# Performance work log

Measured on AMD Instinct MI355X. Metric: run time of the kernel, lower is better.

## Reference

```python
import jax, jax.numpy as jnp
import numpy as np

BATCH = 16384
N_IN = 128
CTX = 128
H = 1024
NB = 8                      # num_bins
OUT_MULT = 3 * NB - 1       # widths + heights + derivatives for RQS
TAIL = 3.0                  # tail_bound
SCALE = float(np.sqrt((H * H) // 2))  # sqrt(prod(hidden_dims)//len(hidden_dims))
MIN_W = 1e-3; MIN_H = 1e-3; MIN_D = 1e-3
DPAD = float(np.log(np.exp(1.0 - MIN_D) - 1.0))  # softplus(DPAD)+MIN_D == 1 at boundaries


def _masks():
    # Standard sequential MADE masks. Input degrees 1..n_in, hidden degrees cycle.
    deg_in = np.arange(1, N_IN + 1)
    deg_h = (np.arange(H) % (N_IN - 1)) + 1
    m0 = deg_h[:, None] >= deg_in[None, :]          # [H, N_IN]
    m1 = deg_h[:, None] >= deg_h[None, :]           # [H, H]
    deg_out = np.repeat(deg_in, OUT_MULT)           # matches view(b, n_in, out_mult)
    m2 = deg_out[:, None] > deg_h[None, :]          # [N_IN*OUT_MULT, H]
    return jnp.asarray(m0), jnp.asarray(m1), jnp.asarray(m2)


def setup_inputs() -> dict:
    key = jax.random.key(0)
    k = jax.random.split(key, 6)
    def rn(kk, shape, fan_in):
        return (jax.random.normal(kk, shape, dtype=jnp.float32) * np.sqrt(1.0 / fan_in)).astype(jnp.float32)
    m0, m1, m2 = _masks()
    return {
        "x": jax.random.normal(k[0], (BATCH, N_IN), dtype=jnp.float32),
        "context": jax.random.normal(k[1], (BATCH, CTX), dtype=jnp.float32),
        "ctx_w": rn(k[2], (H, CTX), CTX),
        "w0": rn(k[3], (H, N_IN), N_IN), "b0": jnp.zeros((H,), jnp.float32),
        "w1": rn(k[4], (H, H), H),       "b1": jnp.zeros((H,), jnp.float32),
        "w2": rn(k[5], (N_IN * OUT_MULT, H), H), "b2": jnp.zeros((N_IN * OUT_MULT,), jnp.float32),
        "mask0": m0, "mask1": m1, "mask2": m2,
    }


def _rqs(x, uw, uh, ud):
    # x: [B, D]; uw, uh: [B, D, NB]; ud: [B, D, NB-1]
    inside = jnp.abs(x) <= TAIL
    xc = jnp.clip(x, -TAIL, TAIL)

    w = MIN_W + (1.0 - MIN_W * NB) * jax.nn.softmax(uw, axis=-1)
    cw = jnp.cumsum(w, axis=-1)
    cw = jnp.concatenate([jnp.zeros_like(cw[..., :1]), cw], axis=-1)
    cw = 2.0 * TAIL * cw - TAIL
    cw = cw.at[..., 0].set(-TAIL).at[..., -1].set(TAIL)
    widths = cw[..., 1:] - cw[..., :-1]

    h = MIN_H + (1.0 - MIN_H * NB) * jax.nn.softmax(uh, axis=-1)
    ch = jnp.cumsum(h, axis=-1)
    ch = jnp.concatenate([jnp.zeros_like(ch[..., :1]), ch], axis=-1)
    ch = 2.0 * TAIL * ch - TAIL
    ch = ch.at[..., 0].set(-TAIL).at[..., -1].set(TAIL)
    heights = ch[..., 1:] - ch[..., :-1]

    pad = jnp.full(ud.shape[:-1] + (1,), DPAD, ud.dtype)
    d = MIN_D + jax.nn.softplus(jnp.concatenate([pad, ud, pad], axis=-1))  # [B, D, NB+1]

    # bucketize: bin index per element (NB is small; comparison-sum beats searchsorted here)
    idx = jnp.clip(jnp.sum((xc[..., None] >= cw).astype(jnp.int32), axis=-1) - 1, 0, NB - 1)
    g = lambda a, i: jnp.take_along_axis(a, i[..., None], axis=-1)[..., 0]

    in_cw = g(cw, idx); in_w = g(widths, idx)
    in_ch = g(ch, idx); in_h = g(heights, idx)
    delta = in_h / in_w
    d0 = g(d, idx); d1 = g(d, idx + 1)

    theta = (xc - in_cw) / in_w
    t1m = theta * (1.0 - theta)
    denom = delta + (d0 + d1 - 2.0 * delta) * t1m
    num = in_h * (delta * theta * theta + d0 * t1m)
    y = in_ch + num / denom
    logdet = (2.0 * jnp.log(delta)
              + jnp.log(d1 * theta * theta + 2.0 * delta * t1m + d0 * (1.0 - theta) ** 2)
              - 2.0 * jnp.log(denom))

    y = jnp.where(inside, y, x)          # identity linear tails
    logdet = jnp.where(inside, logdet, 0.0)
    return y, logdet


def reference(x, context, ctx_w, w0, b0, w1, b1, w2, b2, mask0, mask1, mask2):
    m0 = mask0.astype(w0.dtype); m1 = mask1.astype(w1.dtype); m2 = mask2.astype(w2.dtype)
    hdn = jax.nn.relu(context @ ctx_w.T + x @ (w0 * m0).T + b0)
    hdn = jax.nn.relu(hdn @ (w1 * m1).T + b1)
    out = (hdn @ (w2 * m2).T + b2).reshape(-1, N_IN, OUT_MULT)
    uw = out[..., :NB] / SCALE
    uh = out[..., NB:2 * NB] / SCALE
    ud = out[..., 2 * NB:]
    y, ld = _rqs(x, uw, uh, ud)
    return y, jnp.sum(ld, axis=-1)
```

## Files before the change

### kernel.cpp

```cpp
#include <hip/hip_runtime.h>
#include <cstdint>
#include <cstddef>

#define BATCH   16384
#define N_IN    128
#define CTX     128
#define HDIM    1024
#define NB      8
#define OUT_MULT 23
#define OUT_PAD 24
#define NOUTP   (N_IN * OUT_PAD)
#define KCAT    (CTX + N_IN)

typedef __bf16 bf16x8 __attribute__((ext_vector_type(8)));
typedef float  f32x4  __attribute__((ext_vector_type(4)));

__device__ __forceinline__ uint16_t f2bf(float f) {
    union { float f; uint32_t u; } v; v.f = f;
    uint32_t u = v.u;
    u += 0x7FFFu + ((u >> 16) & 1u);
    return (uint16_t)(u >> 16);
}

__device__ __forceinline__ int kpref_dev(int d) {
    return (d <= 8) ? 9 * d : 72 + 8 * (d - 8);
}
__device__ __forceinline__ int dpos_dev(int p) {
    return (p < 72) ? (p / 9) : (8 + ((p - 72) >> 3));
}
__device__ __forceinline__ int h_of(int p) {
    if (p < 72) { int d = p / 9, j = p - 9 * d; return d + 127 * j; }
    int q = p - 72; int d = 8 + (q >> 3); int j = q & 7; return d + 127 * j;
}

__device__ __forceinline__ void async_ld16(const void* g, const void* l) {
    __builtin_amdgcn_global_load_lds(
        (__attribute__((address_space(1))) void*)(uintptr_t)g,
        (__attribute__((address_space(3))) void*)(uint32_t)(uintptr_t)l,
        16, 0, 0);
}


__global__ void pack_all(
    const float* __restrict__ x,    const float* __restrict__ ctx,
    const float* __restrict__ ctx_w,const float* __restrict__ w0,
    const float* __restrict__ b0,   const float* __restrict__ w1,
    const float* __restrict__ b1,   const float* __restrict__ w2,
    const float* __restrict__ b2,
    uint16_t* __restrict__ xcat, uint16_t* __restrict__ wcat,
    uint16_t* __restrict__ w1m,  uint16_t* __restrict__ w2p,
    float* __restrict__ b0p, float* __restrict__ b1p, float* __restrict__ b2p,
    float* __restrict__ ldz)
{
    const int blk = blockIdx.x;
    const int tid = threadIdx.x;
    if (blk < 16384) {
        int idx = blk * 256 + tid;
        int b = idx >> 8, c = idx & 255;
        float v = (c < CTX) ? ctx[(b << 7) + c] : x[(b << 7) + (c - CTX)];
        xcat[idx] = f2bf(v);
    } else if (blk < 17408) {
        int idx = (blk - 16384) * 256 + tid;
        int p = idx >> 8, c = idx & 255;
        int h = h_of(p);
        float v;
        if (c < CTX) v = ctx_w[(h << 7) + c];
        else {
            int col = c - CTX;
            v = (dpos_dev(p) >= col) ? w0[(h << 7) + col] : 0.0f;
        }
        wcat[idx] = f2bf(v);
    } else if (blk < 21504) {
        int idx = (blk - 17408) * 256 + tid;
        int po = idx >> 10, pi = idx & 1023;
        float v = (dpos_dev(po) >= dpos_dev(pi))
                ? w1[h_of(po) * HDIM + h_of(pi)] : 0.0f;
        w1m[idx] = f2bf(v);
    } else if (blk < 33792) {
        int idx = (blk - 21504) * 256 + tid;
        int oo = idx >> 10, pi = idx & 1023;
        int g = oo / OUT_PAD, t = oo - g * OUT_PAD;
        float v = (t < OUT_MULT && g > dpos_dev(pi))
                ? w2[(g * OUT_MULT + t) * HDIM + h_of(pi)] : 0.0f;
        w2p[idx] = f2bf(v);
    } else if (blk < 33808) {
        int idx = (blk - 33792) * 256 + tid;
        if (idx < HDIM) {
            int h = h_of(idx);
            b0p[idx] = b0[h];
            b1p[idx] = b1[h];
        } else {
            int oo = idx - HDIM;
            int g = oo / OUT_PAD, t = oo - g * OUT_PAD;
            b2p[oo] = (t < OUT_MULT) ? b2[g * OUT_MULT + t] : 0.0f;
        }
    } else {
        int idx = (blk - 33808) * 256 + tid;
        ldz[idx] = 0.0f;
    }
}


template<int MODE>
__global__ __launch_bounds__(256, 2) void gemm_bt(
    const uint16_t* __restrict__ A,
    const uint16_t* __restrict__ B,
    const float*    __restrict__ bias,
    uint16_t*       __restrict__ C,
    int N, int K, int NT)
{
    __shared__ __align__(16) uint16_t sA[128 * 32];
    __shared__ __align__(16) uint16_t sB[128 * 32];

    const int GM    = 64;
    const int per   = GM * NT;
    const int id    = blockIdx.x;
    const int grp   = id / per;
    const int rem   = id - grp * per;
    const int mt    = grp * GM + (rem & (GM - 1));
    const int nt    = rem >> 6;
    const int bm    = mt << 7;
    const int bn    = nt << 7;

    int K_eff;
    if (MODE == 0)      { int dmax = dpos_dev(bn + 127); K_eff = 128 + dmax + 1; }
    else                { int dmax = dpos_dev(bn + 127); K_eff = kpref_dev(dmax + 1); }
    K_eff = min(K, (K_eff + 31) & ~31);

    const int tid   = threadIdx.x;
    const int wid   = tid >> 6;
    const int lane  = tid & 63;
    const int wm    = (wid & 1) << 6;
    const int wn    = (wid >> 1) << 6;
    const int lrow  = lane & 15;
    const int lquad = lane >> 4;

    const f32x4 vzero = {0.0f, 0.0f, 0.0f, 0.0f};
    f32x4 acc[4][4];
#pragma unroll
    for (int i = 0; i < 4; ++i)
#pragma unroll
        for (int j = 0; j < 4; ++j) acc[i][j] = vzero;

    const int c0 = (wid << 6) + lane;
    const int c1 = c0 + 256;
    const char* gA = (const char*)(A + (size_t)bm * K);
    const char* gB = (const char*)(B + (size_t)bn * K);
    const size_t ga0 = (size_t)(c0 >> 2) * K * 2 + (size_t)(c0 & 3) * 16;
    const size_t ga1 = (size_t)(c1 >> 2) * K * 2 + (size_t)(c1 & 3) * 16;
    const char* lA0 = (const char*)sA + (size_t)(wid << 6) * 16;
    const char* lA1 = lA0 + 256 * 16;
    const char* lB0 = (const char*)sB + (size_t)(wid << 6) * 16;
    const char* lB1 = lB0 + 256 * 16;

    const uint16_t* rA = sA + (wm + lrow) * 32 + lquad * 8;
    const uint16_t* rB = sB + (wn + lrow) * 32 + lquad * 8;

    for (int k0 = 0; k0 < K_eff; k0 += 32) {
        __syncthreads();
        const size_t kb = (size_t)k0 * 2;
        async_ld16(gA + ga0 + kb, lA0);
        async_ld16(gA + ga1 + kb, lA1);
        async_ld16(gB + ga0 + kb, lB0);
        async_ld16(gB + ga1 + kb, lB1);
        __syncthreads();

        bf16x8 af[4], bfr[4];
#pragma unroll
        for (int i = 0; i < 4; ++i) af[i]  = *(const bf16x8*)(rA + i * 16 * 32);
#pragma unroll
        for (int j = 0; j < 4; ++j) bfr[j] = *(const bf16x8*)(rB + j * 16 * 32);
#pragma unroll
        for (int i = 0; i < 4; ++i)
#pragma unroll
            for (int j = 0; j < 4; ++j)
                acc[i][j] = __builtin_amdgcn_mfma_f32_16x16x32_bf16(
                                af[i], bfr[j], acc[i][j], 0, 0, 0);
    }

#pragma unroll
    for (int j = 0; j < 4; ++j) {
        const int col = bn + wn + j * 16 + lrow;
        const float bv = bias[col];
#pragma unroll
        for (int i = 0; i < 4; ++i) {
            const int row0 = bm + wm + i * 16 + (lquad << 2);
#pragma unroll
            for (int r = 0; r < 4; ++r) {
                float v = fmaxf(acc[i][j][r] + bv, 0.0f);
                C[(size_t)(row0 + r) * N + col] = f2bf(v);
            }
        }
    }
}


__device__ __forceinline__ float frcp(float v) { return __builtin_amdgcn_rcpf(v); }
__device__ __forceinline__ float softplusf(float v) {
    return fmaxf(v, 0.0f) + __logf(1.0f + __expf(-fabsf(v)));
}

__device__ __forceinline__ void spline_eval(const float* __restrict__ pp,
                                            float xv, float& yout, float& ldout)
{
    float p[OUT_MULT];
#pragma unroll
    for (int k = 0; k < OUT_MULT; ++k) p[k] = pp[k];

    const float TAILF = 3.0f;
    const float MIN_W = 0.001f, MIN_H = 0.001f, MIN_D = 0.001f;
    const float INV_SCALE = 1.0f / 724.0773439350246f;

    const float xc = fminf(fmaxf(xv, -TAILF), TAILF);

    float uw[NB], uh[NB];
#pragma unroll
    for (int k = 0; k < NB; ++k) { uw[k] = p[k] * INV_SCALE; uh[k] = p[NB + k] * INV_SCALE; }
    float mw = uw[0], mh = uh[0];
#pragma unroll
    for (int k = 1; k < NB; ++k) { mw = fmaxf(mw, uw[k]); mh = fmaxf(mh, uh[k]); }
    float ew[NB], eh[NB], sw = 0.0f, sh = 0.0f;
#pragma unroll
    for (int k = 0; k < NB; ++k) {
        ew[k] = __expf(uw[k] - mw); sw += ew[k];
        eh[k] = __expf(uh[k] - mh); sh += eh[k];
    }
    const float FACW = (1.0f - MIN_W * NB) * frcp(sw);
    const float FACH = (1.0f - MIN_H * NB) * frcp(sh);

    float cw[NB + 1], ch[NB + 1];
    cw[0] = -TAILF; ch[0] = -TAILF;
    float aw = 0.0f, ah = 0.0f;
#pragma unroll
    for (int k = 0; k < NB; ++k) {
        aw += MIN_W + FACW * ew[k];
        ah += MIN_H + FACH * eh[k];
        cw[k + 1] = (k == NB - 1) ? TAILF : 2.0f * TAILF * aw - TAILF;
        ch[k + 1] = (k == NB - 1) ? TAILF : 2.0f * TAILF * ah - TAILF;
    }

    float dd[NB + 1];
    dd[0]  = 1.0f;
    dd[NB] = 1.0f;
#pragma unroll
    for (int k = 1; k < NB; ++k) dd[k] = MIN_D + softplusf(p[2 * NB + (k - 1)]);

    float in_cw = cw[0], cw_n = cw[1], in_ch = ch[0], ch_n = ch[1];
    float d0 = dd[0], d1 = dd[1];
#pragma unroll
    for (int k = 1; k < NB; ++k) {
        const bool ge = (xc >= cw[k]);
        in_cw = ge ? cw[k]     : in_cw;
        cw_n  = ge ? cw[k + 1] : cw_n;
        in_ch = ge ? ch[k]     : in_ch;
        ch_n  = ge ? ch[k + 1] : ch_n;
        d0    = ge ? dd[k]     : d0;
        d1    = ge ? dd[k + 1] : d1;
    }
    const float in_w  = cw_n - in_cw;
    const float in_h  = ch_n - in_ch;
    const float inv_w = frcp(in_w);
    const float delta = in_h * inv_w;
    const float theta = (xc - in_cw) * inv_w;
    const float omt   = 1.0f - theta;
    const float t1m   = theta * omt;
    const float denom = delta + (d0 + d1 - 2.0f * delta) * t1m;
    const float num   = in_h * (delta * theta * theta + d0 * t1m);
    float yv = in_ch + num * frcp(denom);
    float ld = 2.0f * __logf(delta)
             + __logf(d1 * theta * theta + 2.0f * delta * t1m + d0 * omt * omt)
             - 2.0f * __logf(denom);
    const bool inside = fabsf(xv) <= TAILF;
    yout  = inside ? yv : xv;
    ldout = inside ? ld : 0.0f;
}


__global__ __launch_bounds__(256, 2) void gemm3_spline(
    const uint16_t* __restrict__ A,
    const uint16_t* __restrict__ B,
    const float*    __restrict__ bias,
    const float*    __restrict__ x,
    float* __restrict__ y,
    float* __restrict__ ldsum)
{
    __shared__ __align__(16) char smem[64 * 97 * 4];
    uint16_t* sA = (uint16_t*)smem;
    uint16_t* sB = (uint16_t*)(smem + 8192);
    float* ep    = (float*)smem;

    const int NT  = 32;
    const int per = 64 * NT;
    const int id  = blockIdx.x;
    const int grp = id / per;
    const int rem = id - grp * per;
    const int mt  = grp * 64 + (rem & 63);
    const int nt  = rem >> 6;
    const int bm  = mt << 7;
    const int bn  = nt * 96;

    const int K = HDIM;
    int K_eff = kpref_dev(4 * nt + 3);
    K_eff = min(K, (K_eff + 31) & ~31);

    const int tid   = threadIdx.x;
    const int wid   = tid >> 6;
    const int lane  = tid & 63;
    const int wm    = (wid & 1) << 6;
    const int wn    = (wid >> 1) * 48;
    const int lrow  = lane & 15;
    const int lquad = lane >> 4;

    const f32x4 vzero = {0.0f, 0.0f, 0.0f, 0.0f};
    f32x4 acc[4][3];
#pragma unroll
    for (int i = 0; i < 4; ++i)
#pragma unroll
        for (int j = 0; j < 3; ++j) acc[i][j] = vzero;

    const int cA0 = (wid << 6) + lane;
    const int cA1 = cA0 + 256;
    const int cB1 = 256 + (wid << 6) + lane;
    const char* gA = (const char*)(A + (size_t)bm * K);
    const char* gB = (const char*)(B + (size_t)bn * K);
    const size_t gaA0 = (size_t)(cA0 >> 2) * K * 2 + (size_t)(cA0 & 3) * 16;
    const size_t gaA1 = (size_t)(cA1 >> 2) * K * 2 + (size_t)(cA1 & 3) * 16;
    const size_t gaB0 = gaA0;
    const size_t gaB1 = (size_t)(cB1 >> 2) * K * 2 + (size_t)(cB1 & 3) * 16;
    const char* lA0 = (const char*)sA + (size_t)(wid << 6) * 16;
    const char* lA1 = lA0 + 256 * 16;
    const char* lB0 = (const char*)sB + (size_t)(wid << 6) * 16;
    const char* lB1 = (const char*)sB + 4096 + (size_t)(wid << 6) * 16;

    const uint16_t* rA = sA + (wm + lrow) * 32 + lquad * 8;
    const uint16_t* rB = sB + (wn + lrow) * 32 + lquad * 8;

    for (int k0 = 0; k0 < K_eff; k0 += 32) {
        __syncthreads();
        const size_t kb = (size_t)k0 * 2;
        async_ld16(gA + gaA0 + kb, lA0);
        async_ld16(gA + gaA1 + kb, lA1);
        async_ld16(gB + gaB0 + kb, lB0);
        if (wid < 2) async_ld16(gB + gaB1 + kb, lB1);
        __syncthreads();

        bf16x8 af[4], bfr[3];
#pragma unroll
        for (int i = 0; i < 4; ++i) af[i]  = *(const bf16x8*)(rA + i * 16 * 32);
#pragma unroll
        for (int j = 0; j < 3; ++j) bfr[j] = *(const bf16x8*)(rB + j * 16 * 32);
#pragma unroll
        for (int i = 0; i < 4; ++i)
#pragma unroll
            for (int j = 0; j < 3; ++j)
                acc[i][j] = __builtin_amdgcn_mfma_f32_16x16x32_bf16(
                                af[i], bfr[j], acc[i][j], 0, 0, 0);
    }

    const int srow = tid >> 2;
    const int sg   = tid & 3;
#pragma unroll
    for (int e = 0; e < 2; ++e) {
        __syncthreads();
        if (wm == (e << 6)) {
#pragma unroll
            for (int j = 0; j < 3; ++j) {
                const int col = wn + j * 16 + lrow;
                const float bv = bias[bn + col];
#pragma unroll
                for (int i = 0; i < 4; ++i) {
                    const int r0 = i * 16 + (lquad << 2);
#pragma unroll
                    for (int r = 0; r < 4; ++r)
                        ep[(r0 + r) * 97 + col] = acc[i][j][r] + bv;
                }
            }
        }
        __syncthreads();

        const int grow = bm + (e << 6) + srow;
        const float xv = x[(size_t)grow * N_IN + (4 * nt + sg)];
        float yv, ld;
        spline_eval(ep + srow * 97 + sg * OUT_PAD, xv, yv, ld);
        y[(size_t)grow * N_IN + 4 * nt + sg] = yv;

        ld += __shfl_xor(ld, 1, 64);
        ld += __shfl_xor(ld, 2, 64);
        if (sg == 0) atomicAdd(&ldsum[grow], ld);
    }
}


extern "C" void kernel_launch(void* const* d_in, const int* in_sizes, int n_in,
                              void* d_out, int out_size, void* d_ws, size_t ws_size,
                              hipStream_t stream)
{
    const float* x     = (const float*)d_in[0];
    const float* ctx   = (const float*)d_in[1];
    const float* ctx_w = (const float*)d_in[2];
    const float* w0    = (const float*)d_in[3];
    const float* b0    = (const float*)d_in[4];
    const float* w1    = (const float*)d_in[5];
    const float* b1    = (const float*)d_in[6];
    const float* w2    = (const float*)d_in[7];
    const float* b2    = (const float*)d_in[8];

    char* ws = (char*)d_ws;
    const size_t XCAT_B = (size_t)BATCH * KCAT * 2;
    const size_t H_B    = (size_t)BATCH * HDIM * 2;
    const size_t WCAT_B = (size_t)HDIM * KCAT * 2;
    const size_t W1_B   = (size_t)HDIM * HDIM * 2;
    const size_t W2P_B  = (size_t)NOUTP * HDIM * 2;

    uint16_t* xcat = (uint16_t*)(ws);
    uint16_t* h1   = (uint16_t*)(ws + XCAT_B);
    uint16_t* h2   = (uint16_t*)(ws + XCAT_B + H_B);
    uint16_t* wcat = (uint16_t*)(ws + XCAT_B + 2 * H_B);
    uint16_t* w1m  = (uint16_t*)(ws + XCAT_B + 2 * H_B + WCAT_B);
    uint16_t* w2p  = (uint16_t*)(ws + XCAT_B + 2 * H_B + WCAT_B + W1_B);
    float*    b0p  = (float*)   (ws + XCAT_B + 2 * H_B + WCAT_B + W1_B + W2P_B);
    float*    b1p  = b0p + HDIM;
    float*    b2p  = b1p + HDIM;

    float* yout  = (float*)d_out;
    float* ldout = yout + (size_t)BATCH * N_IN;

    pack_all<<<33872, 256, 0, stream>>>(x, ctx, ctx_w, w0, b0, w1, b1, w2, b2,
                                        xcat, wcat, w1m, w2p, b0p, b1p, b2p,
                                        ldout);

    const dim3 blk(256);
    gemm_bt<0><<<dim3(128 * (HDIM / 128)), blk, 0, stream>>>(
        xcat, wcat, b0p, h1, HDIM, KCAT, HDIM / 128);
    gemm_bt<1><<<dim3(128 * (HDIM / 128)), blk, 0, stream>>>(
        h1, w1m, b1p, h2, HDIM, HDIM, HDIM / 128);
    gemm3_spline<<<dim3(128 * 32), blk, 0, stream>>>(
        h2, w2p, b2p, x, yout, ldout);
}
```

Measured before the change: 247.9 us.

## Double K-tile depth to 64 with XOR-swizzled LDS layout in GEMM kernels

Both GEMM kernels now stage a 64-wide K slice per iteration instead of 32, which halves the number of barrier pairs and global-to-LDS load rounds. The LDS rows are laid out with an XOR swizzle of the 16-byte chunk index by row, so the fragment reads avoid bank conflicts. The cost is doubled LDS per block and K_eff rounded up to a multiple of 64, which may add some wasted MFMA work on masked-prefix tiles.

```diff
diff --git a/kernel.cpp b/kernel.cpp
--- a/kernel.cpp
+++ b/kernel.cpp
@@ -109,8 +109,8 @@
     uint16_t*       __restrict__ C,
     int N, int K, int NT)
 {
-    __shared__ __align__(16) uint16_t sA[128 * 32];
-    __shared__ __align__(16) uint16_t sB[128 * 32];
+    __shared__ __align__(16) uint16_t sA[128 * 64];
+    __shared__ __align__(16) uint16_t sB[128 * 64];
 
     const int GM    = 64;
     const int per   = GM * NT;
@@ -125,7 +125,7 @@
     int K_eff;
     if (MODE == 0)      { int dmax = dpos_dev(bn + 127); K_eff = 128 + dmax + 1; }
     else                { int dmax = dpos_dev(bn + 127); K_eff = kpref_dev(dmax + 1); }
-    K_eff = min(K, (K_eff + 31) & ~31);
+    K_eff = min(K, (K_eff + 63) & ~63);
 
     const int tid   = threadIdx.x;
     const int wid   = tid >> 6;
@@ -142,40 +142,47 @@
 #pragma unroll
         for (int j = 0; j < 4; ++j) acc[i][j] = vzero;
 
-    const int c0 = (wid << 6) + lane;
-    const int c1 = c0 + 256;
+    int goff[4];
+#pragma unroll
+    for (int t = 0; t < 4; ++t) {
+        int c = t * 256 + tid;
+        int row = c >> 3, j = c & 7;
+        int oct = j ^ (row & 7);
+        goff[t] = row * K * 2 + oct * 16;
+    }
     const char* gA = (const char*)(A + (size_t)bm * K);
     const char* gB = (const char*)(B + (size_t)bn * K);
-    const size_t ga0 = (size_t)(c0 >> 2) * K * 2 + (size_t)(c0 & 3) * 16;
-    const size_t ga1 = (size_t)(c1 >> 2) * K * 2 + (size_t)(c1 & 3) * 16;
-    const char* lA0 = (const char*)sA + (size_t)(wid << 6) * 16;
-    const char* lA1 = lA0 + 256 * 16;
-    const char* lB0 = (const char*)sB + (size_t)(wid << 6) * 16;
-    const char* lB1 = lB0 + 256 * 16;
-
-    const uint16_t* rA = sA + (wm + lrow) * 32 + lquad * 8;
-    const uint16_t* rB = sB + (wn + lrow) * 32 + lquad * 8;
-
-    for (int k0 = 0; k0 < K_eff; k0 += 32) {
-        __syncthreads();
-        const size_t kb = (size_t)k0 * 2;
-        async_ld16(gA + ga0 + kb, lA0);
-        async_ld16(gA + ga1 + kb, lA1);
-        async_ld16(gB + ga0 + kb, lB0);
-        async_ld16(gB + ga1 + kb, lB1);
-        __syncthreads();
-
-        bf16x8 af[4], bfr[4];
-#pragma unroll
-        for (int i = 0; i < 4; ++i) af[i]  = *(const bf16x8*)(rA + i * 16 * 32);
-#pragma unroll
-        for (int j = 0; j < 4; ++j) bfr[j] = *(const bf16x8*)(rB + j * 16 * 32);
-#pragma unroll
-        for (int i = 0; i < 4; ++i)
-#pragma unroll
-            for (int j = 0; j < 4; ++j)
-                acc[i][j] = __builtin_amdgcn_mfma_f32_16x16x32_bf16(
-                                af[i], bfr[j], acc[i][j], 0, 0, 0);
+
+    const int octx = lrow & 7;
+    const uint16_t* rA = sA + (wm + lrow) * 64;
+    const uint16_t* rB = sB + (wn + lrow) * 64;
+
+    for (int k0 = 0; k0 < K_eff; k0 += 64) {
+        __syncthreads();
+        const int kb = k0 * 2;
+#pragma unroll
+        for (int t = 0; t < 4; ++t) {
+            const int ldsoff = (t * 256 + (wid << 6)) * 16;
+            async_ld16(gA + goff[t] + kb, (const char*)sA + ldsoff);
+            async_ld16(gB + goff[t] + kb, (const char*)sB + ldsoff);
+        }
+        __syncthreads();
+
+#pragma unroll
+        for (int ks = 0; ks < 2; ++ks) {
+            const int oct = ((ks << 2) | lquad) ^ octx;
+            bf16x8 af[4], bfr[4];
+#pragma unroll
+            for (int i = 0; i < 4; ++i) af[i]  = *(const bf16x8*)(rA + i * 1024 + oct * 8);
+#pragma unroll
+            for (int j = 0; j < 4; ++j) bfr[j] = *(const bf16x8*)(rB + j * 1024 + oct * 8);
+#pragma unroll
+            for (int i = 0; i < 4; ++i)
+#pragma unroll
+                for (int j = 0; j < 4; ++j)
+                    acc[i][j] = __builtin_amdgcn_mfma_f32_16x16x32_bf16(
+                                    af[i], bfr[j], acc[i][j], 0, 0, 0);
+        }
     }
 
 #pragma unroll
@@ -284,9 +291,9 @@
     float* __restrict__ y,
     float* __restrict__ ldsum)
 {
-    __shared__ __align__(16) char smem[64 * 97 * 4];
+    __shared__ __align__(16) char smem[128 * 64 * 2 + 96 * 64 * 2];
     uint16_t* sA = (uint16_t*)smem;
-    uint16_t* sB = (uint16_t*)(smem + 8192);
+    uint16_t* sB = (uint16_t*)(smem + 16384);
     float* ep    = (float*)smem;
 
     const int NT  = 32;
@@ -301,7 +308,7 @@
 
     const int K = HDIM;
     int K_eff = kpref_dev(4 * nt + 3);
-    K_eff = min(K, (K_eff + 31) & ~31);
+    K_eff = min(K, (K_eff + 63) & ~63);
 
     const int tid   = threadIdx.x;
     const int wid   = tid >> 6;
@@ -318,43 +325,53 @@
 #pragma unroll
         for (int j = 0; j < 3; ++j) acc[i][j] = vzero;
 
-    const int cA0 = (wid << 6) + lane;
-    const int cA1 = cA0 + 256;
-    const int cB1 = 256 + (wid << 6) + lane;
+    int goffA[4], goffB[3];
+#pragma unroll
+    for (int t = 0; t < 4; ++t) {
+        int c = t * 256 + tid;
+        int row = c >> 3, j = c & 7;
+        goffA[t] = row * K * 2 + (j ^ (row & 7)) * 16;
+    }
+#pragma unroll
+    for (int t = 0; t < 3; ++t) {
+        int c = t * 256 + tid;
+        int row = c >> 3, j = c & 7;
+        goffB[t] = row * K * 2 + (j ^ (row & 7)) * 16;
+    }
     const char* gA = (const char*)(A + (size_t)bm * K);
     const char* gB = (const char*)(B + (size_t)bn * K);
-    const size_t gaA0 = (size_t)(cA0 >> 2) * K * 2 + (size_t)(cA0 & 3) * 16;
-    const size_t gaA1 = (size_t)(cA1 >> 2) * K * 2 + (size_t)(cA1 & 3) * 16;
-    const size_t gaB0 = gaA0;
-    const size_t gaB1 = (size_t)(cB1 >> 2) * K * 2 + (size_t)(cB1 & 3) * 16;
-    const char* lA0 = (const char*)sA + (size_t)(wid << 6) * 16;
-    const char* lA1 = lA0 + 256 * 16;
-    const char* lB0 = (const char*)sB + (size_t)(wid << 6) * 16;
-    const char* lB1 = (const char*)sB + 4096 + (size_t)(wid << 6) * 16;
-
-    const uint16_t* rA = sA + (wm + lrow) * 32 + lquad * 8;
-    const uint16_t* rB = sB + (wn + lrow) * 32 + lquad * 8;
-
-    for (int k0 = 0; k0 < K_eff; k0 += 32) {
-        __syncthreads();
-        const size_t kb = (size_t)k0 * 2;
-        async_ld16(gA + gaA0 + kb, lA0);
-        async_ld16(gA + gaA1 + kb, lA1);
-        async_ld16(gB + gaB0 + kb, lB0);
-        if (wid < 2) async_ld16(gB + gaB1 + kb, lB1);
-        __syncthreads();
-
-        bf16x8 af[4], bfr[3];
-#pragma unroll
-        for (int i = 0; i < 4; ++i) af[i]  = *(const bf16x8*)(rA + i * 16 * 32);
-#pragma unroll
-        for (int j = 0; j < 3; ++j) bfr[j] = *(const bf16x8*)(rB + j * 16 * 32);
-#pragma unroll
-        for (int i = 0; i < 4; ++i)
-#pragma unroll
-            for (int j = 0; j < 3; ++j)
-                acc[i][j] = __builtin_amdgcn_mfma_f32_16x16x32_bf16(
-                                af[i], bfr[j], acc[i][j], 0, 0, 0);
+
+    const int octx = lrow & 7;
+    const uint16_t* rA = sA + (wm + lrow) * 64;
+    const uint16_t* rB = sB + (wn + lrow) * 64;
+
+    for (int k0 = 0; k0 < K_eff; k0 += 64) {
+        __syncthreads();
+        const int kb = k0 * 2;
+#pragma unroll
+        for (int t = 0; t < 4; ++t) {
+            const int ldsoff = (t * 256 + (wid << 6)) * 16;
+            async_ld16(gA + goffA[t] + kb, (const char*)sA + ldsoff);
+            if (t < 3)
+                async_ld16(gB + goffB[t] + kb, (const char*)sB + ldsoff);
+        }
+        __syncthreads();
+
+#pragma unroll
+        for (int ks = 0; ks < 2; ++ks) {
+            const int oct = ((ks << 2) | lquad) ^ octx;
+            bf16x8 af[4], bfr[3];
+#pragma unroll
+            for (int i = 0; i < 4; ++i) af[i]  = *(const bf16x8*)(rA + i * 1024 + oct * 8);
+#pragma unroll
+            for (int j = 0; j < 3; ++j) bfr[j] = *(const bf16x8*)(rB + j * 1024 + oct * 8);
+#pragma unroll
+            for (int i = 0; i < 4; ++i)
+#pragma unroll
+                for (int j = 0; j < 3; ++j)
+                    acc[i][j] = __builtin_amdgcn_mfma_f32_16x16x32_bf16(
+                                    af[i], bfr[j], acc[i][j], 0, 0, 0);
+        }
     }
 
     const int srow = tid >> 2;
```

New measurement: 241.1 us. -2.8%, faster.
